# Kernel optimization log

Measured on AMD Instinct MI355X. Metric: run time of the kernel, lower is better.

Reference implementation:

```python
import jax, jax.numpy as jnp
import numpy as np

# 4-neighborhood from init_kwargs: offsets (dr, dc) of each neighbor
NEIGHBORHOOD = ((0, 1), (1, 0), (0, -1), (-1, 0))
B, C, H, W = 8, 8, 512, 512
STEPS = 10


def setup_inputs() -> dict:
    key = jax.random.key(0)
    k1, k2, k3 = jax.random.split(key, 3)
    unaries = jax.random.normal(k1, (B, C, H, W), jnp.float32)
    binaries = jax.random.normal(k2, (len(NEIGHBORHOOD), C, C), jnp.float32)
    sample = jax.random.randint(k3, (B, H, W), 0, C, dtype=jnp.int32)
    return {"unaries": unaries, "binaries": binaries, "sample": sample,
            "sample_steps": STEPS}


def _shift(x, dr, dc):
    # value at (r, c) becomes x[r+dr, c+dc] (wrap; wrapped entries are masked out)
    return jnp.roll(x, (-dr, -dc), axis=(-2, -1))


def _valid_mask(h, w, dr, dc):
    r = jnp.arange(h)[:, None]
    c = jnp.arange(w)[None, :]
    return (r + dr >= 0) & (r + dr < h) & (c + dc >= 0) & (c + dc < w)


def reference(unaries, binaries, sample, sample_steps):
    b, nc, h, w = unaries.shape
    masks = [_valid_mask(h, w, dr, dc) for dr, dc in NEIGHBORHOOD]  # each [H,W]

    def energies(s):
        # total energy per candidate label: unary + sum_n binaries[n, label, nb_label]
        e = unaries
        for n, (dr, dc) in enumerate(NEIGHBORHOOD):
            nb = _shift(s, dr, dc)                              # [B,H,W] int
            contrib = binaries[n][:, nb]                        # [C,B,H,W]
            contrib = jnp.transpose(contrib, (1, 0, 2, 3))      # [B,C,H,W]
            e = e + jnp.where(masks[n][None, None], contrib, jnp.float32(0))
        return e

    def step(carry, k):
        s, acc = carry
        logits = -energies(s)                                   # lower energy -> higher prob
        probs = jax.nn.softmax(logits, axis=1)                  # [B,C,H,W]
        g = jax.random.gumbel(k, logits.shape, logits.dtype)
        s_new = jnp.argmax(logits + g, axis=1).astype(s.dtype)  # Gibbs categorical draw
        return (s_new, acc + probs), None

    keys = jax.random.split(jax.random.key(42), sample_steps)
    (s_final, acc), _ = jax.lax.scan(step, (sample, jnp.zeros_like(unaries)), keys)
    sample_result = acc / jnp.float32(sample_steps)             # per-class marginal estimate
    return sample_result, s_final
```

## Files before the change

kernel.cpp:

```cpp
#include <hip/hip_runtime.h>
#include <stdint.h>
#include <math.h>

constexpr int Wd = 512;
constexpr int Hd = 512;
constexpr int Cd = 8;
constexpr int Bd = 8;
constexpr int HW = Hd * Wd;
constexpr int CHW = Cd * HW;
constexpr int BCHW = Bd * CHW;
constexpr int BHW = Bd * HW;
constexpr int NT = 256;

constexpr float LN2 = 0.69314718055994530942f;

__device__ __forceinline__ float fast_ln(float x) {
  return __builtin_amdgcn_logf(x) * LN2;
}

__host__ __device__ __forceinline__ void tf2x32(uint32_t k0, uint32_t k1,
                                                uint32_t x0, uint32_t x1,
                                                uint32_t& o0, uint32_t& o1) {
  const uint32_t k2 = k0 ^ k1 ^ 0x1BD11BDAu;
  x0 += k0; x1 += k1;
#define TFR(r) { x0 += x1; x1 = (x1 << (r)) | (x1 >> (32 - (r))); x1 ^= x0; }
  TFR(13) TFR(15) TFR(26) TFR(6)
  x0 += k1; x1 += k2 + 1u;
  TFR(17) TFR(29) TFR(16) TFR(24)
  x0 += k2; x1 += k0 + 2u;
  TFR(13) TFR(15) TFR(26) TFR(6)
  x0 += k0; x1 += k1 + 3u;
  TFR(17) TFR(29) TFR(16) TFR(24)
  x0 += k1; x1 += k2 + 4u;
  TFR(13) TFR(15) TFR(26) TFR(6)
  x0 += k2; x1 += k0 + 5u;
#undef TFR
  o0 = x0; o1 = x1;
}

__device__ __forceinline__ void fill_sb(float* sb, const float* binaries) {
  for (int i = threadIdx.x; i < 288; i += NT) {
    const int n = i / 72, rem = i - n * 72;
    const int ch = rem / 9, nb = rem - ch * 9;
    sb[i] = (nb < 8) ? binaries[n * 64 + ch * 8 + nb] : 0.0f;
  }
}

__device__ __forceinline__ void energies(const float* __restrict__ u,
                                         const float* sb, int i0, int i1,
                                         int i2, int i3, float* e) {
#pragma unroll
  for (int ch = 0; ch < 8; ++ch) {
    float v = u[ch];
    v += sb[      ch * 9 + i0];
    v += sb[ 72 + ch * 9 + i1];
    v += sb[144 + ch * 9 + i2];
    v += sb[216 + ch * 9 + i3];
    e[ch] = v;
  }
}

__device__ __forceinline__ int gumbel_argmax(const float* e, int ub,
                                             uint32_t k0, uint32_t k1) {
  float zbest = 0.0f;
  int amax = 0;
#pragma unroll
  for (int ch = 0; ch < 8; ++ch) {
    uint32_t y0, y1;
    tf2x32(k0, k1, 0u, (uint32_t)(ub + ch * HW), y0, y1);
    const uint32_t bits = y0 ^ y1;
    const float f = __uint_as_float((bits >> 9) | 0x3F800000u) - 1.0f;
    const float U = (f > 0.0f) ? f : 1.17549435082228751e-38f;
    const float l1 = fast_ln(U);
    const float gum = -fast_ln(-l1);
    const float z = gum - e[ch];
    if (ch == 0 || z > zbest) { zbest = z; amax = ch; }
  }
  return amax;
}

template <int FIRST, int LAST>
__global__ __launch_bounds__(NT) void traj_step(
    const float* __restrict__ unaries, const float* __restrict__ binaries,
    const int* __restrict__ s0_int, const uint8_t* __restrict__ s_in,
    uint8_t* __restrict__ s_out, float* __restrict__ sfin,
    uint32_t k0, uint32_t k1) {
  __shared__ float sb[288];
  fill_sb(sb, binaries);
  __syncthreads();

  const int tid = blockIdx.x * NT + threadIdx.x;
  const int c = tid & (Wd - 1);
  const int r = (tid >> 9) & (Hd - 1);
  const int b = tid >> 18;
  const int site = tid & (HW - 1);

  int i0, i1, i2, i3;
  if (FIRST) {
    i0 = (c + 1) < Wd ? s0_int[tid + 1]  : 8;
    i1 = (r + 1) < Hd ? s0_int[tid + Wd] : 8;
    i2 = c > 0        ? s0_int[tid - 1]  : 8;
    i3 = r > 0        ? s0_int[tid - Wd] : 8;
  } else {
    i0 = (c + 1) < Wd ? (int)s_in[tid + 1]  : 8;
    i1 = (r + 1) < Hd ? (int)s_in[tid + Wd] : 8;
    i2 = c > 0        ? (int)s_in[tid - 1]  : 8;
    i3 = r > 0        ? (int)s_in[tid - Wd] : 8;
  }

  const int ub = b * CHW + site;
  float u[8];
#pragma unroll
  for (int ch = 0; ch < 8; ++ch) u[ch] = unaries[ub + ch * HW];
  float e[8];
  energies(u, sb, i0, i1, i2, i3, e);

  const int amax = gumbel_argmax(e, ub, k0, k1);

  if (LAST) sfin[tid] = (float)amax;
  else      s_out[tid] = (uint8_t)amax;
}

__global__ __launch_bounds__(NT) void prob_pass(
    const float* __restrict__ unaries, const float* __restrict__ binaries,
    const int* __restrict__ s0_int, const uint8_t* __restrict__ sbufs,
    float* __restrict__ acc_out) {
  __shared__ float sb[288];
  fill_sb(sb, binaries);
  __syncthreads();

  const int tid = blockIdx.x * NT + threadIdx.x;
  const int c = tid & (Wd - 1);
  const int r = (tid >> 9) & (Hd - 1);
  const int b = tid >> 18;
  const int site = tid & (HW - 1);
  const bool v0 = (c + 1) < Wd, v1 = (r + 1) < Hd, v2 = c > 0, v3 = r > 0;

  const int ub = b * CHW + site;
  float u[8];
#pragma unroll
  for (int ch = 0; ch < 8; ++ch) u[ch] = unaries[ub + ch * HW];

  float acc[8] = {};

#pragma unroll 1
  for (int t = 0; t < 10; ++t) {
    int i0, i1, i2, i3;
    if (t == 0) {
      i0 = v0 ? s0_int[tid + 1]  : 8;
      i1 = v1 ? s0_int[tid + Wd] : 8;
      i2 = v2 ? s0_int[tid - 1]  : 8;
      i3 = v3 ? s0_int[tid - Wd] : 8;
    } else {
      const uint8_t* s = sbufs + (size_t)(t - 1) * BHW;
      i0 = v0 ? (int)s[tid + 1]  : 8;
      i1 = v1 ? (int)s[tid + Wd] : 8;
      i2 = v2 ? (int)s[tid - 1]  : 8;
      i3 = v3 ? (int)s[tid - Wd] : 8;
    }

    float e[8];
    energies(u, sb, i0, i1, i2, i3, e);

    float m = -e[0];
#pragma unroll
    for (int ch = 1; ch < 8; ++ch) m = fmaxf(m, -e[ch]);
    float p[8];
    float s = 0.0f;
#pragma unroll
    for (int ch = 0; ch < 8; ++ch) { p[ch] = __expf(-e[ch] - m); s += p[ch]; }
    const float inv = __builtin_amdgcn_rcpf(s);
#pragma unroll
    for (int ch = 0; ch < 8; ++ch) acc[ch] += p[ch] * inv;
  }

#pragma unroll
  for (int ch = 0; ch < 8; ++ch) acc_out[ub + ch * HW] = acc[ch] * 0.1f;
}

__global__ __launch_bounds__(NT) void gibbs_step(
    const float* __restrict__ unaries, const float* __restrict__ binaries,
    const int* __restrict__ s_in, int* __restrict__ s_out,
    float* __restrict__ acc, float* __restrict__ sfin,
    uint32_t k0, uint32_t k1, int mode) {
  __shared__ float sb[288];
  fill_sb(sb, binaries);
  __syncthreads();

  const int tid = blockIdx.x * NT + threadIdx.x;
  const int c = tid & (Wd - 1);
  const int r = (tid >> 9) & (Hd - 1);
  const int b = tid >> 18;
  const int i0 = (c + 1) < Wd ? s_in[tid + 1]  : 8;
  const int i1 = (r + 1) < Hd ? s_in[tid + Wd] : 8;
  const int i2 = c > 0        ? s_in[tid - 1]  : 8;
  const int i3 = r > 0        ? s_in[tid - Wd] : 8;

  const int ub = b * CHW + (tid & (HW - 1));
  float u[8];
#pragma unroll
  for (int ch = 0; ch < 8; ++ch) u[ch] = unaries[ub + ch * HW];
  float e[8];
  energies(u, sb, i0, i1, i2, i3, e);

  const int amax = gumbel_argmax(e, ub, k0, k1);

  float m = -e[0];
#pragma unroll
  for (int ch = 1; ch < 8; ++ch) m = fmaxf(m, -e[ch]);
  float p[8];
  float s = 0.0f;
#pragma unroll
  for (int ch = 0; ch < 8; ++ch) { p[ch] = __expf(-e[ch] - m); s += p[ch]; }
  const float inv = __builtin_amdgcn_rcpf(s);

  if (mode == 0) {
#pragma unroll
    for (int ch = 0; ch < 8; ++ch) acc[ub + ch * HW] = p[ch] * inv;
  } else if (mode == 1) {
#pragma unroll
    for (int ch = 0; ch < 8; ++ch) acc[ub + ch * HW] += p[ch] * inv;
  } else {
#pragma unroll
    for (int ch = 0; ch < 8; ++ch) {
      const int ix = ub + ch * HW;
      acc[ix] = (acc[ix] + p[ch] * inv) * 0.1f;
    }
  }

  if (mode != 2) s_out[tid] = amax;
  else sfin[tid] = (float)amax;
}

extern "C" void kernel_launch(void* const* d_in, const int* in_sizes, int n_in,
                              void* d_out, int out_size, void* d_ws, size_t ws_size,
                              hipStream_t stream) {
  const float* unaries  = (const float*)d_in[0];
  const float* binaries = (const float*)d_in[1];
  const int*   sample0  = (const int*)d_in[2];

  float* acc_out = (float*)d_out;
  float* sfin = acc_out + BCHW;

  uint32_t ka[10], kb[10];
  for (int t = 0; t < 10; ++t)
    tf2x32(0u, 42u, 0u, (uint32_t)t, ka[t], kb[t]);

  const dim3 grid(BHW / NT), blk(NT);

  if (ws_size >= (size_t)9 * BHW) {
    uint8_t* sbufs = (uint8_t*)d_ws;
    for (int t = 0; t < 10; ++t) {
      const uint8_t* sin = (t == 0) ? nullptr : sbufs + (size_t)(t - 1) * BHW;
      uint8_t* sout = (t == 9) ? nullptr : sbufs + (size_t)t * BHW;
      if (t == 0)
        traj_step<1, 0><<<grid, blk, 0, stream>>>(unaries, binaries, sample0,
                                                  nullptr, sout, sfin, ka[t], kb[t]);
      else if (t == 9)
        traj_step<0, 1><<<grid, blk, 0, stream>>>(unaries, binaries, nullptr,
                                                  sin, nullptr, sfin, ka[t], kb[t]);
      else
        traj_step<0, 0><<<grid, blk, 0, stream>>>(unaries, binaries, nullptr,
                                                  sin, sout, sfin, ka[t], kb[t]);
    }
    prob_pass<<<grid, blk, 0, stream>>>(unaries, binaries, sample0, sbufs,
                                        acc_out);
  } else {
    int* bufA = (int*)d_ws;
    int* bufB = (int*)sfin;
    for (int t = 0; t < 10; ++t) {
      const int* sin = (t == 0) ? sample0 : ((t & 1) ? bufA : bufB);
      int* sout = (t & 1) ? bufB : bufA;
      const int mode = (t == 0) ? 0 : ((t == 9) ? 2 : 1);
      gibbs_step<<<grid, blk, 0, stream>>>(unaries, binaries, sin, sout,
                                           acc_out, sfin, ka[t], kb[t], mode);
    }
  }
}
```

Baseline: 556.3 us.

## Fuse pairs of Gibbs steps into one tiled kernel with halo recompute in LDS

Replaces the ten per-step trajectory kernels with five fused kernels, each running two Gibbs steps on a 16x64 tile. The first step also recomputes a one-cell halo into shared memory, so the second step reads neighbour labels from LDS rather than from global memory. This halves the launches and the global label round-trips. In exchange the halo cells pay extra unary loads and RNG work. The binaries table is also transposed so each neighbour row is fetched with two float4 LDS reads.

```diff
diff --git a/kernel.cpp b/kernel.cpp
--- a/kernel.cpp
+++ b/kernel.cpp
@@ -11,6 +11,11 @@
 constexpr int BCHW = Bd * CHW;
 constexpr int BHW = Bd * HW;
 constexpr int NT = 256;
+
+constexpr int TR = 16, TC = 64;
+constexpr int ER = TR + 2, EC = TC + 2;
+constexpr int ESZ = ER * EC;
+constexpr int TILES = (Hd / TR) * (Wd / TC);
 
 constexpr float LN2 = 0.69314718055994530942f;
 
@@ -60,6 +65,36 @@
   }
 }
 
+__device__ __forceinline__ void fill_sbT(float* sbT, const float* binaries) {
+  for (int i = threadIdx.x; i < 288; i += NT) {
+    const int n = i / 72, rem = i - n * 72;
+    const int ch = rem / 9, nb = rem - ch * 9;
+    sbT[n * 108 + nb * 12 + ch] = (nb < 8) ? binaries[n * 64 + ch * 8 + nb]
+                                           : 0.0f;
+  }
+}
+
+__device__ __forceinline__ void energiesT(const float* __restrict__ u,
+                                          const float* sbT, int i0, int i1,
+                                          int i2, int i3, float* e) {
+  const float4* r0 = (const float4*)(sbT +       i0 * 12);
+  const float4* r1 = (const float4*)(sbT + 108 + i1 * 12);
+  const float4* r2 = (const float4*)(sbT + 216 + i2 * 12);
+  const float4* r3 = (const float4*)(sbT + 324 + i3 * 12);
+  const float4 a0 = r0[0], b0 = r0[1];
+  const float4 a1 = r1[0], b1 = r1[1];
+  const float4 a2 = r2[0], b2 = r2[1];
+  const float4 a3 = r3[0], b3 = r3[1];
+  e[0] = u[0] + a0.x + a1.x + a2.x + a3.x;
+  e[1] = u[1] + a0.y + a1.y + a2.y + a3.y;
+  e[2] = u[2] + a0.z + a1.z + a2.z + a3.z;
+  e[3] = u[3] + a0.w + a1.w + a2.w + a3.w;
+  e[4] = u[4] + b0.x + b1.x + b2.x + b3.x;
+  e[5] = u[5] + b0.y + b1.y + b2.y + b3.y;
+  e[6] = u[6] + b0.z + b1.z + b2.z + b3.z;
+  e[7] = u[7] + b0.w + b1.w + b2.w + b3.w;
+}
+
 __device__ __forceinline__ int gumbel_argmax(const float* e, int ub,
                                              uint32_t k0, uint32_t k1) {
   float zbest = 0.0f;
@@ -80,53 +115,88 @@
 }
 
 template <int FIRST, int LAST>
-__global__ __launch_bounds__(NT) void traj_step(
+__global__ __launch_bounds__(NT, 8) void traj_fused(
     const float* __restrict__ unaries, const float* __restrict__ binaries,
-    const int* __restrict__ s0_int, const uint8_t* __restrict__ s_in,
-    uint8_t* __restrict__ s_out, float* __restrict__ sfin,
-    uint32_t k0, uint32_t k1) {
-  __shared__ float sb[288];
-  fill_sb(sb, binaries);
+    const int* __restrict__ s0_int, const uint8_t* __restrict__ sprev,
+    uint8_t* __restrict__ soutA, uint8_t* __restrict__ soutB,
+    float* __restrict__ sfin,
+    uint32_t k0a, uint32_t k1a, uint32_t k0b, uint32_t k1b) {
+  __shared__ __align__(16) float sbT[432];
+  __shared__ uint8_t lab[ESZ];
+  fill_sbT(sbT, binaries);
   __syncthreads();
 
-  const int tid = blockIdx.x * NT + threadIdx.x;
-  const int c = tid & (Wd - 1);
-  const int r = (tid >> 9) & (Hd - 1);
-  const int b = tid >> 18;
-  const int site = tid & (HW - 1);
-
-  int i0, i1, i2, i3;
-  if (FIRST) {
-    i0 = (c + 1) < Wd ? s0_int[tid + 1]  : 8;
-    i1 = (r + 1) < Hd ? s0_int[tid + Wd] : 8;
-    i2 = c > 0        ? s0_int[tid - 1]  : 8;
-    i3 = r > 0        ? s0_int[tid - Wd] : 8;
-  } else {
-    i0 = (c + 1) < Wd ? (int)s_in[tid + 1]  : 8;
-    i1 = (r + 1) < Hd ? (int)s_in[tid + Wd] : 8;
-    i2 = c > 0        ? (int)s_in[tid - 1]  : 8;
-    i3 = r > 0        ? (int)s_in[tid - Wd] : 8;
-  }
-
-  const int ub = b * CHW + site;
-  float u[8];
-#pragma unroll
-  for (int ch = 0; ch < 8; ++ch) u[ch] = unaries[ub + ch * HW];
-  float e[8];
-  energies(u, sb, i0, i1, i2, i3, e);
-
-  const int amax = gumbel_argmax(e, ub, k0, k1);
-
-  if (LAST) sfin[tid] = (float)amax;
-  else      s_out[tid] = (uint8_t)amax;
+  const int b    = blockIdx.x >> 8;
+  const int tile = blockIdx.x & 255;
+  const int tr   = (tile >> 3) << 4;
+  const int tc   = (tile & 7) << 6;
+  const int base = b * HW;
+
+#pragma unroll 1
+  for (int k = 0; k < 5; ++k) {
+    const int s = threadIdx.x + k * NT;
+    if (s < ESZ) {
+      const int er = s / EC, ec = s - er * EC;
+      const int r = tr + er - 1, c = tc + ec - 1;
+      if ((unsigned)r < (unsigned)Hd && (unsigned)c < (unsigned)Wd) {
+        const int g = base + (r << 9) + c;
+        int i0, i1, i2, i3;
+        if (FIRST) {
+          i0 = (c + 1) < Wd ? s0_int[g + 1]  : 8;
+          i1 = (r + 1) < Hd ? s0_int[g + Wd] : 8;
+          i2 = c > 0        ? s0_int[g - 1]  : 8;
+          i3 = r > 0        ? s0_int[g - Wd] : 8;
+        } else {
+          i0 = (c + 1) < Wd ? (int)sprev[g + 1]  : 8;
+          i1 = (r + 1) < Hd ? (int)sprev[g + Wd] : 8;
+          i2 = c > 0        ? (int)sprev[g - 1]  : 8;
+          i3 = r > 0        ? (int)sprev[g - Wd] : 8;
+        }
+        const int ub = b * CHW + (r << 9) + c;
+        float u[8];
+#pragma unroll
+        for (int ch = 0; ch < 8; ++ch) u[ch] = unaries[ub + ch * HW];
+        float e[8];
+        energiesT(u, sbT, i0, i1, i2, i3, e);
+        const int amax = gumbel_argmax(e, ub, k0a, k1a);
+        lab[s] = (uint8_t)amax;
+        if (er >= 1 && er < (ER - 1) && ec >= 1 && ec < (EC - 1))
+          soutA[g] = (uint8_t)amax;
+      }
+    }
+  }
+  __syncthreads();
+
+#pragma unroll 1
+  for (int k = 0; k < 4; ++k) {
+    const int s = threadIdx.x + k * NT;
+    const int ir = s >> 6, ic = s & 63;
+    const int er = ir + 1, ec = ic + 1;
+    const int r = tr + ir, c = tc + ic;
+    const int g = base + (r << 9) + c;
+    const int ls = er * EC + ec;
+    const int i0 = (c + 1) < Wd ? (int)lab[ls + 1]  : 8;
+    const int i1 = (r + 1) < Hd ? (int)lab[ls + EC] : 8;
+    const int i2 = c > 0        ? (int)lab[ls - 1]  : 8;
+    const int i3 = r > 0        ? (int)lab[ls - EC] : 8;
+    const int ub = b * CHW + (r << 9) + c;
+    float u[8];
+#pragma unroll
+    for (int ch = 0; ch < 8; ++ch) u[ch] = unaries[ub + ch * HW];
+    float e[8];
+    energiesT(u, sbT, i0, i1, i2, i3, e);
+    const int amax = gumbel_argmax(e, ub, k0b, k1b);
+    if (LAST) sfin[g] = (float)amax;
+    else      soutB[g] = (uint8_t)amax;
+  }
 }
 
 __global__ __launch_bounds__(NT) void prob_pass(
     const float* __restrict__ unaries, const float* __restrict__ binaries,
     const int* __restrict__ s0_int, const uint8_t* __restrict__ sbufs,
     float* __restrict__ acc_out) {
-  __shared__ float sb[288];
-  fill_sb(sb, binaries);
+  __shared__ __align__(16) float sbT[432];
+  fill_sbT(sbT, binaries);
   __syncthreads();
 
   const int tid = blockIdx.x * NT + threadIdx.x;
@@ -160,7 +230,7 @@
     }
 
     float e[8];
-    energies(u, sb, i0, i1, i2, i3, e);
+    energiesT(u, sbT, i0, i1, i2, i3, e);
 
     float m = -e[0];
 #pragma unroll
@@ -246,28 +316,37 @@
   for (int t = 0; t < 10; ++t)
     tf2x32(0u, 42u, 0u, (uint32_t)t, ka[t], kb[t]);
 
-  const dim3 grid(BHW / NT), blk(NT);
+  const dim3 blk(NT);
 
   if (ws_size >= (size_t)9 * BHW) {
     uint8_t* sbufs = (uint8_t*)d_ws;
-    for (int t = 0; t < 10; ++t) {
-      const uint8_t* sin = (t == 0) ? nullptr : sbufs + (size_t)(t - 1) * BHW;
-      uint8_t* sout = (t == 9) ? nullptr : sbufs + (size_t)t * BHW;
-      if (t == 0)
-        traj_step<1, 0><<<grid, blk, 0, stream>>>(unaries, binaries, sample0,
-                                                  nullptr, sout, sfin, ka[t], kb[t]);
-      else if (t == 9)
-        traj_step<0, 1><<<grid, blk, 0, stream>>>(unaries, binaries, nullptr,
-                                                  sin, nullptr, sfin, ka[t], kb[t]);
+    const dim3 fgrid(Bd * TILES);
+
+    for (int L = 0; L < 5; ++L) {
+      const int tA = 2 * L;
+      const uint8_t* sprev = (L == 0) ? nullptr
+                                      : sbufs + (size_t)(tA - 1) * BHW;
+      uint8_t* soutA = sbufs + (size_t)tA * BHW;
+      uint8_t* soutB = (L == 4) ? nullptr : sbufs + (size_t)(tA + 1) * BHW;
+      if (L == 0)
+        traj_fused<1, 0><<<fgrid, blk, 0, stream>>>(
+            unaries, binaries, sample0, nullptr, soutA, soutB, sfin,
+            ka[tA], kb[tA], ka[tA + 1], kb[tA + 1]);
+      else if (L == 4)
+        traj_fused<0, 1><<<fgrid, blk, 0, stream>>>(
+            unaries, binaries, nullptr, sprev, soutA, nullptr, sfin,
+            ka[tA], kb[tA], ka[tA + 1], kb[tA + 1]);
       else
-        traj_step<0, 0><<<grid, blk, 0, stream>>>(unaries, binaries, nullptr,
-                                                  sin, sout, sfin, ka[t], kb[t]);
-    }
-    prob_pass<<<grid, blk, 0, stream>>>(unaries, binaries, sample0, sbufs,
-                                        acc_out);
+        traj_fused<0, 0><<<fgrid, blk, 0, stream>>>(
+            unaries, binaries, nullptr, sprev, soutA, soutB, sfin,
+            ka[tA], kb[tA], ka[tA + 1], kb[tA + 1]);
+    }
+    prob_pass<<<dim3(BHW / NT), blk, 0, stream>>>(unaries, binaries, sample0,
+                                                  sbufs, acc_out);
   } else {
     int* bufA = (int*)d_ws;
     int* bufB = (int*)sfin;
+    const dim3 grid(BHW / NT);
     for (int t = 0; t < 10; ++t) {
       const int* sin = (t == 0) ? sample0 : ((t & 1) ? bufA : bufB);
       int* sout = (t & 1) ? bufB : bufA;
```

Measured after the change: 719.3 us. 1.29x slower.

## Pack unaries per-site, transpose binary table for vector LDS reads, use exp2

Applied to the files above, without the earlier changes.

Adds a pre-pass that repacks unaries from channel-planar into per-site 8-float records so every step reads them with two float4 loads. The binary table in shared memory is transposed so each neighbor's row can be fetched with float4 reads instead of eight scalar gathers. Neighbor label loads become unconditional with padded workspace offsets, softmax uses exp2 with a folded log2e FMA, the Threefry rotate uses a builtin, and launch bounds request higher occupancy. The cost is an extra pack kernel plus extra workspace traffic, and the packed layout only runs when the workspace is large enough.

```diff
diff --git a/kernel.cpp b/kernel.cpp
--- a/kernel.cpp
+++ b/kernel.cpp
@@ -13,6 +13,7 @@
 constexpr int NT = 256;
 
 constexpr float LN2 = 0.69314718055994530942f;
+constexpr float L2E = 1.44269504088896340736f;
 
 __device__ __forceinline__ float fast_ln(float x) {
   return __builtin_amdgcn_logf(x) * LN2;
@@ -23,7 +24,7 @@
                                                 uint32_t& o0, uint32_t& o1) {
   const uint32_t k2 = k0 ^ k1 ^ 0x1BD11BDAu;
   x0 += k0; x1 += k1;
-#define TFR(r) { x0 += x1; x1 = (x1 << (r)) | (x1 >> (32 - (r))); x1 ^= x0; }
+#define TFR(r) { x0 += x1; x1 = __builtin_rotateleft32(x1, (r)); x1 ^= x0; }
   TFR(13) TFR(15) TFR(26) TFR(6)
   x0 += k1; x1 += k2 + 1u;
   TFR(17) TFR(29) TFR(16) TFR(24)
@@ -60,6 +61,36 @@
   }
 }
 
+__device__ __forceinline__ void fill_sbT(float* sbT, const float* binaries) {
+  for (int i = threadIdx.x; i < 288; i += NT) {
+    const int n = i / 72, rem = i - n * 72;
+    const int ch = rem / 9, nb = rem - ch * 9;
+    sbT[n * 108 + nb * 12 + ch] = (nb < 8) ? binaries[n * 64 + ch * 8 + nb]
+                                           : 0.0f;
+  }
+}
+
+__device__ __forceinline__ void energiesT(const float* __restrict__ u,
+                                          const float* sbT, int i0, int i1,
+                                          int i2, int i3, float* e) {
+  const float4* r0 = (const float4*)(sbT +       i0 * 12);
+  const float4* r1 = (const float4*)(sbT + 108 + i1 * 12);
+  const float4* r2 = (const float4*)(sbT + 216 + i2 * 12);
+  const float4* r3 = (const float4*)(sbT + 324 + i3 * 12);
+  const float4 a0 = r0[0], b0 = r0[1];
+  const float4 a1 = r1[0], b1 = r1[1];
+  const float4 a2 = r2[0], b2 = r2[1];
+  const float4 a3 = r3[0], b3 = r3[1];
+  e[0] = u[0] + a0.x + a1.x + a2.x + a3.x;
+  e[1] = u[1] + a0.y + a1.y + a2.y + a3.y;
+  e[2] = u[2] + a0.z + a1.z + a2.z + a3.z;
+  e[3] = u[3] + a0.w + a1.w + a2.w + a3.w;
+  e[4] = u[4] + b0.x + b1.x + b2.x + b3.x;
+  e[5] = u[5] + b0.y + b1.y + b2.y + b3.y;
+  e[6] = u[6] + b0.z + b1.z + b2.z + b3.z;
+  e[7] = u[7] + b0.w + b1.w + b2.w + b3.w;
+}
+
 __device__ __forceinline__ int gumbel_argmax(const float* e, int ub,
                                              uint32_t k0, uint32_t k1) {
   float zbest = 0.0f;
@@ -79,54 +110,33 @@
   return amax;
 }
 
-template <int FIRST, int LAST>
-__global__ __launch_bounds__(NT) void traj_step(
-    const float* __restrict__ unaries, const float* __restrict__ binaries,
+__global__ __launch_bounds__(NT, 8) void pack_unaries(
+    const float* __restrict__ unaries, float* __restrict__ upk) {
+  const int tid = blockIdx.x * NT + threadIdx.x;
+  const int b = tid >> 18;
+  const int site = tid & (HW - 1);
+  const int ub = b * CHW + site;
+  float4 x, y;
+  x.x = unaries[ub];
+  x.y = unaries[ub +     HW];
+  x.z = unaries[ub + 2 * HW];
+  x.w = unaries[ub + 3 * HW];
+  y.x = unaries[ub + 4 * HW];
+  y.y = unaries[ub + 5 * HW];
+  y.z = unaries[ub + 6 * HW];
+  y.w = unaries[ub + 7 * HW];
+  float4* up = (float4*)(upk + ((size_t)tid << 3));
+  up[0] = x; up[1] = y;
+}
+
+template <int FIRST, int LAST, int UPACK>
+__global__ __launch_bounds__(NT, 8) void traj_step(
+    const float* __restrict__ U, const float* __restrict__ binaries,
     const int* __restrict__ s0_int, const uint8_t* __restrict__ s_in,
     uint8_t* __restrict__ s_out, float* __restrict__ sfin,
     uint32_t k0, uint32_t k1) {
-  __shared__ float sb[288];
-  fill_sb(sb, binaries);
-  __syncthreads();
-
-  const int tid = blockIdx.x * NT + threadIdx.x;
-  const int c = tid & (Wd - 1);
-  const int r = (tid >> 9) & (Hd - 1);
-  const int b = tid >> 18;
-  const int site = tid & (HW - 1);
-
-  int i0, i1, i2, i3;
-  if (FIRST) {
-    i0 = (c + 1) < Wd ? s0_int[tid + 1]  : 8;
-    i1 = (r + 1) < Hd ? s0_int[tid + Wd] : 8;
-    i2 = c > 0        ? s0_int[tid - 1]  : 8;
-    i3 = r > 0        ? s0_int[tid - Wd] : 8;
-  } else {
-    i0 = (c + 1) < Wd ? (int)s_in[tid + 1]  : 8;
-    i1 = (r + 1) < Hd ? (int)s_in[tid + Wd] : 8;
-    i2 = c > 0        ? (int)s_in[tid - 1]  : 8;
-    i3 = r > 0        ? (int)s_in[tid - Wd] : 8;
-  }
-
-  const int ub = b * CHW + site;
-  float u[8];
-#pragma unroll
-  for (int ch = 0; ch < 8; ++ch) u[ch] = unaries[ub + ch * HW];
-  float e[8];
-  energies(u, sb, i0, i1, i2, i3, e);
-
-  const int amax = gumbel_argmax(e, ub, k0, k1);
-
-  if (LAST) sfin[tid] = (float)amax;
-  else      s_out[tid] = (uint8_t)amax;
-}
-
-__global__ __launch_bounds__(NT) void prob_pass(
-    const float* __restrict__ unaries, const float* __restrict__ binaries,
-    const int* __restrict__ s0_int, const uint8_t* __restrict__ sbufs,
-    float* __restrict__ acc_out) {
-  __shared__ float sb[288];
-  fill_sb(sb, binaries);
+  __shared__ __align__(16) float sbT[432];
+  fill_sbT(sbT, binaries);
   __syncthreads();
 
   const int tid = blockIdx.x * NT + threadIdx.x;
@@ -136,10 +146,68 @@
   const int site = tid & (HW - 1);
   const bool v0 = (c + 1) < Wd, v1 = (r + 1) < Hd, v2 = c > 0, v3 = r > 0;
 
+  int i0, i1, i2, i3;
+  if (FIRST) {
+    i0 = v0 ? s0_int[tid + 1]  : 8;
+    i1 = v1 ? s0_int[tid + Wd] : 8;
+    i2 = v2 ? s0_int[tid - 1]  : 8;
+    i3 = v3 ? s0_int[tid - Wd] : 8;
+  } else {
+    const uint8_t* sp = s_in + tid;
+    const int n0 = sp[1], n1 = sp[Wd], n2 = sp[-1], n3 = sp[-Wd];
+    i0 = v0 ? n0 : 8;
+    i1 = v1 ? n1 : 8;
+    i2 = v2 ? n2 : 8;
+    i3 = v3 ? n3 : 8;
+  }
+
   const int ub = b * CHW + site;
   float u[8];
-#pragma unroll
-  for (int ch = 0; ch < 8; ++ch) u[ch] = unaries[ub + ch * HW];
+  if (UPACK) {
+    const float4* up = (const float4*)(U + ((size_t)tid << 3));
+    const float4 x = up[0], y = up[1];
+    u[0] = x.x; u[1] = x.y; u[2] = x.z; u[3] = x.w;
+    u[4] = y.x; u[5] = y.y; u[6] = y.z; u[7] = y.w;
+  } else {
+#pragma unroll
+    for (int ch = 0; ch < 8; ++ch) u[ch] = U[ub + ch * HW];
+  }
+  float e[8];
+  energiesT(u, sbT, i0, i1, i2, i3, e);
+
+  const int amax = gumbel_argmax(e, ub, k0, k1);
+
+  if (LAST) sfin[tid] = (float)amax;
+  else      s_out[tid] = (uint8_t)amax;
+}
+
+template <int UPACK>
+__global__ __launch_bounds__(NT, 8) void prob_pass(
+    const float* __restrict__ U, const float* __restrict__ binaries,
+    const int* __restrict__ s0_int, const uint8_t* __restrict__ sbufs,
+    float* __restrict__ acc_out) {
+  __shared__ __align__(16) float sbT[432];
+  fill_sbT(sbT, binaries);
+  __syncthreads();
+
+  const int tid = blockIdx.x * NT + threadIdx.x;
+  const int c = tid & (Wd - 1);
+  const int r = (tid >> 9) & (Hd - 1);
+  const int b = tid >> 18;
+  const int site = tid & (HW - 1);
+  const bool v0 = (c + 1) < Wd, v1 = (r + 1) < Hd, v2 = c > 0, v3 = r > 0;
+
+  const int ub = b * CHW + site;
+  float u[8];
+  if (UPACK) {
+    const float4* up = (const float4*)(U + ((size_t)tid << 3));
+    const float4 x = up[0], y = up[1];
+    u[0] = x.x; u[1] = x.y; u[2] = x.z; u[3] = x.w;
+    u[4] = y.x; u[5] = y.y; u[6] = y.z; u[7] = y.w;
+  } else {
+#pragma unroll
+    for (int ch = 0; ch < 8; ++ch) u[ch] = U[ub + ch * HW];
+  }
 
   float acc[8] = {};
 
@@ -152,23 +220,28 @@
       i2 = v2 ? s0_int[tid - 1]  : 8;
       i3 = v3 ? s0_int[tid - Wd] : 8;
     } else {
-      const uint8_t* s = sbufs + (size_t)(t - 1) * BHW;
-      i0 = v0 ? (int)s[tid + 1]  : 8;
-      i1 = v1 ? (int)s[tid + Wd] : 8;
-      i2 = v2 ? (int)s[tid - 1]  : 8;
-      i3 = v3 ? (int)s[tid - Wd] : 8;
+      const uint8_t* sp = sbufs + (size_t)(t - 1) * BHW + tid;
+      const int n0 = sp[1], n1 = sp[Wd], n2 = sp[-1], n3 = sp[-Wd];
+      i0 = v0 ? n0 : 8;
+      i1 = v1 ? n1 : 8;
+      i2 = v2 ? n2 : 8;
+      i3 = v3 ? n3 : 8;
     }
 
     float e[8];
-    energies(u, sb, i0, i1, i2, i3, e);
+    energiesT(u, sbT, i0, i1, i2, i3, e);
 
     float m = -e[0];
 #pragma unroll
     for (int ch = 1; ch < 8; ++ch) m = fmaxf(m, -e[ch]);
+    const float mm = -m * L2E;
     float p[8];
     float s = 0.0f;
 #pragma unroll
-    for (int ch = 0; ch < 8; ++ch) { p[ch] = __expf(-e[ch] - m); s += p[ch]; }
+    for (int ch = 0; ch < 8; ++ch) {
+      p[ch] = __builtin_amdgcn_exp2f(fmaf(e[ch], -L2E, mm));
+      s += p[ch];
+    }
     const float inv = __builtin_amdgcn_rcpf(s);
 #pragma unroll
     for (int ch = 0; ch < 8; ++ch) acc[ch] += p[ch] * inv;
@@ -232,6 +305,31 @@
   else sfin[tid] = (float)amax;
 }
 
+template <int UPACK>
+static void run_two_pass(const float* U, const float* unaries_orig,
+                         const float* binaries, const int* sample0,
+                         uint8_t* sbufs, float* acc_out, float* sfin,
+                         const uint32_t* ka, const uint32_t* kb,
+                         hipStream_t stream) {
+  const dim3 grid(BHW / NT), blk(NT);
+  for (int t = 0; t < 10; ++t) {
+    const uint8_t* sin = (t == 0) ? nullptr : sbufs + (size_t)(t - 1) * BHW;
+    uint8_t* sout = (t == 9) ? nullptr : sbufs + (size_t)t * BHW;
+    if (t == 0)
+      traj_step<1, 0, UPACK><<<grid, blk, 0, stream>>>(
+          U, binaries, sample0, nullptr, sout, sfin, ka[t], kb[t]);
+    else if (t == 9)
+      traj_step<0, 1, UPACK><<<grid, blk, 0, stream>>>(
+          U, binaries, nullptr, sin, nullptr, sfin, ka[t], kb[t]);
+    else
+      traj_step<0, 0, UPACK><<<grid, blk, 0, stream>>>(
+          U, binaries, nullptr, sin, sout, sfin, ka[t], kb[t]);
+  }
+  prob_pass<UPACK><<<grid, blk, 0, stream>>>(U, binaries, sample0, sbufs,
+                                             acc_out);
+  (void)unaries_orig;
+}
+
 extern "C" void kernel_launch(void* const* d_in, const int* in_sizes, int n_in,
                               void* d_out, int out_size, void* d_ws, size_t ws_size,
                               hipStream_t stream) {
@@ -246,28 +344,25 @@
   for (int t = 0; t < 10; ++t)
     tf2x32(0u, 42u, 0u, (uint32_t)t, ka[t], kb[t]);
 
-  const dim3 grid(BHW / NT), blk(NT);
-
-  if (ws_size >= (size_t)9 * BHW) {
-    uint8_t* sbufs = (uint8_t*)d_ws;
-    for (int t = 0; t < 10; ++t) {
-      const uint8_t* sin = (t == 0) ? nullptr : sbufs + (size_t)(t - 1) * BHW;
-      uint8_t* sout = (t == 9) ? nullptr : sbufs + (size_t)t * BHW;
-      if (t == 0)
-        traj_step<1, 0><<<grid, blk, 0, stream>>>(unaries, binaries, sample0,
-                                                  nullptr, sout, sfin, ka[t], kb[t]);
-      else if (t == 9)
-        traj_step<0, 1><<<grid, blk, 0, stream>>>(unaries, binaries, nullptr,
-                                                  sin, nullptr, sfin, ka[t], kb[t]);
-      else
-        traj_step<0, 0><<<grid, blk, 0, stream>>>(unaries, binaries, nullptr,
-                                                  sin, sout, sfin, ka[t], kb[t]);
-    }
-    prob_pass<<<grid, blk, 0, stream>>>(unaries, binaries, sample0, sbufs,
-                                        acc_out);
+  uint8_t* wsb = (uint8_t*)d_ws;
+  const size_t LAB_OFF  = 512;
+  const size_t need_lab = LAB_OFF + (size_t)9 * BHW + 512;
+  const size_t UPK_OFF  = (need_lab + 255) & ~(size_t)255;
+  const size_t need_pak = UPK_OFF + (size_t)BHW * 8 * sizeof(float);
+  uint8_t* sbufs = wsb + LAB_OFF;
+  float*   upk   = (float*)(wsb + UPK_OFF);
+
+  if (ws_size >= need_pak) {
+    pack_unaries<<<dim3(BHW / NT), dim3(NT), 0, stream>>>(unaries, upk);
+    run_two_pass<1>(upk, unaries, binaries, sample0, sbufs, acc_out, sfin,
+                    ka, kb, stream);
+  } else if (ws_size >= need_lab) {
+    run_two_pass<0>(unaries, unaries, binaries, sample0, sbufs, acc_out, sfin,
+                    ka, kb, stream);
   } else {
     int* bufA = (int*)d_ws;
     int* bufB = (int*)sfin;
+    const dim3 grid(BHW / NT), blk(NT);
     for (int t = 0; t < 10; ++t) {
       const int* sin = (t == 0) ? sample0 : ((t & 1) ? bufA : bufB);
       int* sout = (t & 1) ? bufB : bufA;
```

Result: no change. 565.1 us (+1.6%).
